# Kernel tuning notes

Measured on AMD Instinct MI355X. Metric: run time of the kernel, lower is better.

## Reference

```python
import jax, jax.numpy as jnp
import numpy as np

N_EMBED = 1024
N_HEAD = 16
SEQ = 2048
BATCH = 2


def setup_inputs() -> dict:
    key = jax.random.key(0)
    ks = jax.random.split(key, 5)
    scale_in = 1.0 / np.sqrt(N_EMBED)
    x = jax.random.normal(ks[0], (BATCH, SEQ, N_EMBED), dtype=jnp.float32)
    # attn_proj: Linear(n_embed, 3*n_embed); stored as [in, out] so y = x @ W + b
    W_qkv = jax.random.normal(ks[1], (N_EMBED, 3 * N_EMBED), dtype=jnp.float32) * scale_in
    b_qkv = jax.random.normal(ks[2], (3 * N_EMBED,), dtype=jnp.float32) * 0.01
    # fin_proj: Linear(n_embed, n_embed)
    W_out = jax.random.normal(ks[3], (N_EMBED, N_EMBED), dtype=jnp.float32) * scale_in
    b_out = jax.random.normal(ks[4], (N_EMBED,), dtype=jnp.float32) * 0.01
    return {"x": x, "W_qkv": W_qkv, "b_qkv": b_qkv, "W_out": W_out, "b_out": b_out}


def reference(x, W_qkv, b_qkv, W_out, b_out):
    B, S, D = x.shape
    H = N_HEAD
    hd = D // H
    qkv = x @ W_qkv + b_qkv  # [B, S, 3D]
    q, k, v = jnp.split(qkv, 3, axis=-1)
    # [B, H, S, hd]
    q = q.reshape(B, S, H, hd).transpose(0, 2, 1, 3)
    k = k.reshape(B, S, H, hd).transpose(0, 2, 1, 3)
    v = v.reshape(B, S, H, hd).transpose(0, 2, 1, 3)
    scores = jnp.einsum("bhqd,bhkd->bhqk", q, k) * (1.0 / np.sqrt(hd))
    causal = jnp.tril(jnp.ones((S, S), dtype=bool))  # lower-triangular mask
    scores = jnp.where(causal[None, None], scores, -jnp.inf)
    probs = jax.nn.softmax(scores, axis=-1)
    # dropout is identity in eval mode (inference reference)
    attn = jnp.einsum("bhqk,bhkd->bhqd", probs, v)  # [B, H, S, hd]
    attn = attn.transpose(0, 2, 1, 3).reshape(B, S, D)
    return attn @ W_out + b_out
```

## Files before the change

kernel.cpp:

```cpp
#include <hip/hip_runtime.h>

typedef short bf16x8 __attribute__((ext_vector_type(8)));
typedef short bf16x4 __attribute__((ext_vector_type(4)));
typedef float f32x4 __attribute__((ext_vector_type(4)));
typedef int i32x4 __attribute__((ext_vector_type(4)));
typedef int i32x2 __attribute__((ext_vector_type(2)));

#define MFMA16x16x32(a, b, c) __builtin_amdgcn_mfma_f32_16x16x32_bf16(a, b, c, 0, 0, 0)
#define TRR(dst, a) asm volatile("ds_read_b64_tr_b16 %0, %1" : "=v"(dst) : "v"(a))

__device__ __forceinline__ unsigned short f2bf(float f) {
  union { float f; unsigned u; } v; v.f = f;
  unsigned u = v.u + 0x7FFFu + ((v.u >> 16) & 1u);
  return (unsigned short)(u >> 16);
}

__device__ __forceinline__ unsigned cvtpk(float lo, float hi) {
  unsigned r;
  asm("v_cvt_pk_bf16_f32 %0, %1, %2" : "=v"(r) : "v"(lo), "v"(hi));
  return r;
}

__device__ __forceinline__ float max3f(float a, float b, float c) {
  float d;
  asm("v_max3_f32 %0, %1, %2, %3" : "=v"(d) : "v"(a), "v"(b), "v"(c));
  return d;
}

__device__ __forceinline__ void gload16(const void* g, void* l) {
  __builtin_amdgcn_global_load_lds((const __attribute__((address_space(1))) void*)g,
                                   (__attribute__((address_space(3))) void*)l, 16, 0, 0);
}

__device__ __forceinline__ unsigned ldsoff(const void* p) {
  return (unsigned)(unsigned long long)(const __attribute__((address_space(3))) void*)p;
}

__global__ __launch_bounds__(256) void conv_bf16(const float* __restrict__ in,
                                                 unsigned short* __restrict__ out, int n8) {
  int i = blockIdx.x * 256 + threadIdx.x;
  if (i >= n8) return;
  const float4* p = reinterpret_cast<const float4*>(in + (long)i * 8);
  float4 a = p[0], b = p[1];
  i32x4 o;
  o[0] = cvtpk(a.x, a.y); o[1] = cvtpk(a.z, a.w);
  o[2] = cvtpk(b.x, b.y); o[3] = cvtpk(b.z, b.w);
  *reinterpret_cast<i32x4*>(out + (long)i * 8) = o;
}

__global__ __launch_bounds__(256) void trans_f32_bf16(const float* __restrict__ W,
                                                      unsigned short* __restrict__ Wt,
                                                      int K, int N) {
  __shared__ float tile[32][33];
  int n0 = blockIdx.x << 5, k0 = blockIdx.y << 5;
  int tx = threadIdx.x, ty = threadIdx.y;
#pragma unroll
  for (int i = 0; i < 32; i += 8)
    tile[ty + i][tx] = W[(long)(k0 + ty + i) * N + n0 + tx];
  __syncthreads();
#pragma unroll
  for (int i = 0; i < 32; i += 8)
    Wt[(long)(n0 + ty + i) * K + k0 + tx] = f2bf(tile[tx][ty + i]);
}

template <int BF16OUT>
__global__ __launch_bounds__(256) void gemm_bt(const unsigned short* __restrict__ A,
                                               const unsigned short* __restrict__ Bt,
                                               const float* __restrict__ bias,
                                               void* __restrict__ Cv,
                                               int M, int N, int K) {
  __shared__ __align__(128) unsigned short As[4096];
  __shared__ __align__(128) unsigned short Bs[4096];
  int t = threadIdx.x;
  int w = t >> 6, l = t & 63;
  int g = l >> 4, m16 = l & 15;
  int wr = w >> 1, wc = w & 1;
  long am0 = (long)blockIdx.y << 7;
  long bn0 = (long)blockIdx.x << 7;
  f32x4 acc[4][4];
#pragma unroll
  for (int i = 0; i < 4; ++i)
#pragma unroll
    for (int j = 0; j < 4; ++j) acc[i][j] = (f32x4){0.f, 0.f, 0.f, 0.f};

  for (int k0 = 0; k0 < K; k0 += 32) {
#pragma unroll
    for (int i = 0; i < 2; ++i) {
      int seg = i * 4 + w;
      int flat = (seg << 9) + (l << 3);
      int r_ = flat >> 5, c_ = flat & 31;
      gload16(A + (am0 + r_) * K + k0 + c_, &As[seg << 9]);
      gload16(Bt + (bn0 + r_) * K + k0 + c_, &Bs[seg << 9]);
    }
    __syncthreads();
    bf16x8 af[4], bfr[4];
#pragma unroll
    for (int im = 0; im < 4; ++im)
      af[im] = *(const bf16x8*)&As[((wr << 6) + (im << 4) + m16) * 32 + (g << 3)];
#pragma unroll
    for (int in = 0; in < 4; ++in)
      bfr[in] = *(const bf16x8*)&Bs[((wc << 6) + (in << 4) + m16) * 32 + (g << 3)];
    __builtin_amdgcn_s_setprio(1);
#pragma unroll
    for (int im = 0; im < 4; ++im)
#pragma unroll
      for (int in = 0; in < 4; ++in)
        acc[im][in] = MFMA16x16x32(af[im], bfr[in], acc[im][in]);
    __builtin_amdgcn_s_setprio(0);
    __syncthreads();
  }

#pragma unroll
  for (int im = 0; im < 4; ++im) {
#pragma unroll
    for (int in = 0; in < 4; ++in) {
      long col = bn0 + (wc << 6) + (in << 4) + m16;
      float bval = bias[col];
#pragma unroll
      for (int r = 0; r < 4; ++r) {
        long row = am0 + (wr << 6) + (im << 4) + (g << 2) + r;
        float v = acc[im][in][r] + bval;
        if (BF16OUT)
          ((unsigned short*)Cv)[row * N + col] = f2bf(v);
        else
          ((float*)Cv)[row * N + col] = v;
      }
    }
  }
}

__global__ __launch_bounds__(256) void attn_fwd(const unsigned short* __restrict__ qkv,
                                                unsigned short* __restrict__ out) {
  const int D3 = 3072;
  const float C1 = 0.18033688f;
  const float THR = 11.5415603f;
  __shared__ __align__(128) unsigned short Ks[2][4096];
  __shared__ __align__(128) unsigned short Vs[2][4096];
  int b = blockIdx.x >> 4, h = blockIdx.x & 15;
  int t = threadIdx.x;
  int w = t >> 6, l = t & 63;
  int g = l >> 4, m16 = l & 15;
  long base = (long)b * 2048 * D3;
  const unsigned short* kbase = qkv + base + 1024 + h * 64;
  const unsigned short* vbase = qkv + base + 2048 + h * 64;

  int l8 = l >> 3, sc = l & 7;
  int kof = (w * 8 + l8) * D3 + ((sc ^ l8) << 3);
  int s0 = w * 8 + l8;
  int vof = ((s0 & 15) * 4 + (sc >> 1)) * D3 + ((s0 >> 4) << 4) + ((sc & 1) << 3);
  const f32x4 zero4 = (f32x4){0.f, 0.f, 0.f, 0.f};

  for (int sgi = 0; sgi < 2; ++sgi) {
    int qt = sgi ? (31 - blockIdx.y) : blockIdx.y;
    int q0 = qt << 6;
    int qrow = q0 + (w << 4) + m16;
    const unsigned short* qp = qkv + base + (long)qrow * D3 + h * 64;
    bf16x8 qf0 = *(const bf16x8*)(qp + g * 8);
    bf16x8 qf1 = *(const bf16x8*)(qp + 32 + g * 8);

    f32x4 O[4];
#pragma unroll
    for (int d = 0; d < 4; ++d) O[d] = zero4;
    float m2 = -1e30f, lsum = 0.f;
    int nt = qt + 1;

    gload16(kbase + kof, &Ks[0][w << 9]);
    gload16(kbase + 32 * D3 + kof, &Ks[0][2048 + (w << 9)]);
    gload16(vbase + vof, &Vs[0][w << 9]);
    gload16(vbase + vof + 32, &Vs[0][2048 + (w << 9)]);
    __syncthreads();

    int buf = 0;
    for (int it = 0; it < nt; ++it) {
      if (it + 1 < nt) {
        long off = (long)(it + 1) * 64 * D3;
        gload16(kbase + off + kof, &Ks[buf ^ 1][w << 9]);
        gload16(kbase + off + 32 * D3 + kof, &Ks[buf ^ 1][2048 + (w << 9)]);
        gload16(vbase + off + vof, &Vs[buf ^ 1][w << 9]);
        gload16(vbase + off + vof + 32, &Vs[buf ^ 1][2048 + (w << 9)]);
      }
      unsigned va = ldsoff(&Vs[buf][0]) + (g << 7) + (m16 << 3);
      bf16x4 t0[4], t1[4], t2[4], t3[4];
#pragma unroll
      for (int d = 0; d < 4; ++d) {
        unsigned a = va + (d << 11);
        TRR(t0[d], a);
        TRR(t1[d], a + 512);
        TRR(t2[d], a + 1024);
        TRR(t3[d], a + 1536);
      }
      const char* kbuf = (const char*)&Ks[buf][0];
      int swz = m16 & 7;
      bf16x8 kf0[4], kf1[4];
#pragma unroll
      for (int T = 0; T < 4; ++T) {
        const char* rp = kbuf + (((T << 4) + m16) << 7);
        kf0[T] = *(const bf16x8*)(rp + ((g ^ swz) << 4));
        kf1[T] = *(const bf16x8*)(rp + (((4 + g) ^ swz) << 4));
      }
      f32x4 st[4];
      __builtin_amdgcn_s_setprio(1);
#pragma unroll
      for (int T = 0; T < 4; ++T) {
        st[T] = MFMA16x16x32(kf0[T], qf0, zero4);
        st[T] = MFMA16x16x32(kf1[T], qf1, st[T]);
      }
      __builtin_amdgcn_s_setprio(0);

      if (it == nt - 1) {
        int rq = (w << 4) + m16;
#pragma unroll
        for (int T = 0; T < 4; ++T)
#pragma unroll
          for (int r = 0; r < 4; ++r)
            if ((T << 4) + (g << 2) + r > rq) st[T][r] = -3e38f;
      }
      float tmax = max3f(st[0][0], st[0][1], st[0][2]);
      tmax = max3f(tmax, st[0][3], st[1][0]);
      tmax = max3f(tmax, st[1][1], st[1][2]);
      tmax = max3f(tmax, st[1][3], st[2][0]);
      tmax = max3f(tmax, st[2][1], st[2][2]);
      tmax = max3f(tmax, st[2][3], st[3][0]);
      tmax = max3f(tmax, st[3][1], st[3][2]);
      tmax = fmaxf(tmax, st[3][3]);
      tmax = fmaxf(tmax, __shfl_xor(tmax, 16));
      tmax = fmaxf(tmax, __shfl_xor(tmax, 32));
      float tsc2 = tmax * C1;
      bool skip = __all(tsc2 <= m2 + THR);
      float mnew2 = skip ? m2 : fmaxf(m2, tsc2);
      float p[4][4];
      float tsum = 0.f;
#pragma unroll
      for (int T = 0; T < 4; ++T)
#pragma unroll
        for (int r = 0; r < 4; ++r) {
          float e = __builtin_amdgcn_exp2f(fmaf(st[T][r], C1, -mnew2));
          p[T][r] = e;
          tsum += e;
        }
      tsum += __shfl_xor(tsum, 16);
      tsum += __shfl_xor(tsum, 32);
      if (!skip) {
        float alpha = __builtin_amdgcn_exp2f(m2 - mnew2);
        lsum *= alpha;
#pragma unroll
        for (int d = 0; d < 4; ++d) {
          O[d][0] *= alpha; O[d][1] *= alpha; O[d][2] *= alpha; O[d][3] *= alpha;
        }
        m2 = mnew2;
      }
      lsum += tsum;

      i32x4 w0, w1;
      w0[0] = cvtpk(p[0][0], p[0][1]); w0[1] = cvtpk(p[0][2], p[0][3]);
      w0[2] = cvtpk(p[1][0], p[1][1]); w0[3] = cvtpk(p[1][2], p[1][3]);
      w1[0] = cvtpk(p[2][0], p[2][1]); w1[1] = cvtpk(p[2][2], p[2][3]);
      w1[2] = cvtpk(p[3][0], p[3][1]); w1[3] = cvtpk(p[3][2], p[3][3]);
      bf16x8 pb0 = __builtin_bit_cast(bf16x8, w0);
      bf16x8 pb1 = __builtin_bit_cast(bf16x8, w1);

      asm volatile("s_waitcnt lgkmcnt(0)" ::: "memory");
      __builtin_amdgcn_sched_barrier(0);

      bf16x8 vfA[4], vfB[4];
#pragma unroll
      for (int d = 0; d < 4; ++d) {
        vfA[d] = __builtin_shufflevector(t0[d], t1[d], 0, 1, 2, 3, 4, 5, 6, 7);
        vfB[d] = __builtin_shufflevector(t2[d], t3[d], 0, 1, 2, 3, 4, 5, 6, 7);
      }
      __builtin_amdgcn_s_setprio(1);
#pragma unroll
      for (int d = 0; d < 4; ++d) {
        O[d] = MFMA16x16x32(vfA[d], pb0, O[d]);
        O[d] = MFMA16x16x32(vfB[d], pb1, O[d]);
      }
      __builtin_amdgcn_s_setprio(0);
      __syncthreads();
      buf ^= 1;
    }

    float inv = 1.0f / lsum;
    unsigned short* op = out + (long)(b * 2048 + qrow) * 1024 + h * 64;
#pragma unroll
    for (int d = 0; d < 4; ++d) {
      i32x2 pk;
      pk[0] = (int)cvtpk(O[d][0] * inv, O[d][1] * inv);
      pk[1] = (int)cvtpk(O[d][2] * inv, O[d][3] * inv);
      *reinterpret_cast<i32x2*>(op + (d << 4) + (g << 2)) = pk;
    }
  }
}

extern "C" void kernel_launch(void* const* d_in, const int* in_sizes, int n_in,
                              void* d_out, int out_size, void* d_ws, size_t ws_size,
                              hipStream_t stream) {
  const float* x     = (const float*)d_in[0];
  const float* W_qkv = (const float*)d_in[1];
  const float* b_qkv = (const float*)d_in[2];
  const float* W_out = (const float*)d_in[3];
  const float* b_out = (const float*)d_in[4];

  char* ws = (char*)d_ws;
  unsigned short* xb    = (unsigned short*)ws;
  unsigned short* wqkvT = (unsigned short*)(ws + (8l << 20));
  unsigned short* woutT = (unsigned short*)(ws + (14l << 20));
  unsigned short* qkv   = (unsigned short*)(ws + (16l << 20));

  conv_bf16<<<2048, 256, 0, stream>>>(x, xb, 524288);
  trans_f32_bf16<<<dim3(96, 32), dim3(32, 8), 0, stream>>>(W_qkv, wqkvT, 1024, 3072);
  trans_f32_bf16<<<dim3(32, 32), dim3(32, 8), 0, stream>>>(W_out, woutT, 1024, 1024);
  gemm_bt<1><<<dim3(24, 32), 256, 0, stream>>>(xb, wqkvT, b_qkv, (void*)qkv, 4096, 3072, 1024);
  attn_fwd<<<dim3(32, 16), 256, 0, stream>>>(qkv, xb);
  gemm_bt<0><<<dim3(8, 32), 256, 0, stream>>>(xb, woutT, b_out, d_out, 4096, 1024, 1024);
}
```

Baseline: 119.0 us.

## Widen attention KV tile to 128 keys per iteration

Doubles the key/value tile processed per loop iteration from 64 to 128 rows, with double-buffered shared memory grown to match and the V staging layout changed to suit. This halves the number of iterations and block-wide barriers per query tile and amortizes softmax reductions over more scores. It also sets launch bounds to request two blocks per CU. The costs are more LDS and registers per block, and more masked work on the diagonal tile, since a 64-row query tile now meets a 128-key tile.

```diff
diff --git a/kernel.cpp b/kernel.cpp
--- a/kernel.cpp
+++ b/kernel.cpp
@@ -129,13 +129,13 @@
   }
 }
 
-__global__ __launch_bounds__(256) void attn_fwd(const unsigned short* __restrict__ qkv,
-                                                unsigned short* __restrict__ out) {
+__global__ __launch_bounds__(256, 2) void attn_fwd(const unsigned short* __restrict__ qkv,
+                                                   unsigned short* __restrict__ out) {
   const int D3 = 3072;
   const float C1 = 0.18033688f;
   const float THR = 11.5415603f;
-  __shared__ __align__(128) unsigned short Ks[2][4096];
-  __shared__ __align__(128) unsigned short Vs[2][4096];
+  __shared__ __align__(128) unsigned short Ks[2][8192];
+  __shared__ __align__(128) unsigned short Vs[2][8192];
   int b = blockIdx.x >> 4, h = blockIdx.x & 15;
   int t = threadIdx.x;
   int w = t >> 6, l = t & 63;
@@ -146,8 +146,7 @@
 
   int l8 = l >> 3, sc = l & 7;
   int kof = (w * 8 + l8) * D3 + ((sc ^ l8) << 3);
-  int s0 = w * 8 + l8;
-  int vof = ((s0 & 15) * 4 + (sc >> 1)) * D3 + ((s0 >> 4) << 4) + ((sc & 1) << 3);
+  int vof = ((w * 8 + l8) * 4 + (sc >> 1)) * D3 + ((sc & 1) << 3);
   const f32x4 zero4 = (f32x4){0.f, 0.f, 0.f, 0.f};
 
   for (int sgi = 0; sgi < 2; ++sgi) {
@@ -162,82 +161,80 @@
 #pragma unroll
     for (int d = 0; d < 4; ++d) O[d] = zero4;
     float m2 = -1e30f, lsum = 0.f;
-    int nt = qt + 1;
-
-    gload16(kbase + kof, &Ks[0][w << 9]);
-    gload16(kbase + 32 * D3 + kof, &Ks[0][2048 + (w << 9)]);
-    gload16(vbase + vof, &Vs[0][w << 9]);
-    gload16(vbase + vof + 32, &Vs[0][2048 + (w << 9)]);
+    int nt = (qt >> 1) + 1;
+
+#pragma unroll
+    for (int i = 0; i < 4; ++i) {
+      gload16(kbase + kof + i * 32 * D3, &Ks[0][(i << 11) + (w << 9)]);
+      gload16(vbase + vof + (i << 4), &Vs[0][(i << 11) + (w << 9)]);
+    }
     __syncthreads();
 
     int buf = 0;
     for (int it = 0; it < nt; ++it) {
       if (it + 1 < nt) {
-        long off = (long)(it + 1) * 64 * D3;
-        gload16(kbase + off + kof, &Ks[buf ^ 1][w << 9]);
-        gload16(kbase + off + 32 * D3 + kof, &Ks[buf ^ 1][2048 + (w << 9)]);
-        gload16(vbase + off + vof, &Vs[buf ^ 1][w << 9]);
-        gload16(vbase + off + vof + 32, &Vs[buf ^ 1][2048 + (w << 9)]);
+        long off = (long)(it + 1) * 128 * D3;
+#pragma unroll
+        for (int i = 0; i < 4; ++i) {
+          gload16(kbase + off + kof + i * 32 * D3, &Ks[buf ^ 1][(i << 11) + (w << 9)]);
+          gload16(vbase + off + vof + (i << 4), &Vs[buf ^ 1][(i << 11) + (w << 9)]);
+        }
       }
       unsigned va = ldsoff(&Vs[buf][0]) + (g << 7) + (m16 << 3);
-      bf16x4 t0[4], t1[4], t2[4], t3[4];
-#pragma unroll
-      for (int d = 0; d < 4; ++d) {
-        unsigned a = va + (d << 11);
-        TRR(t0[d], a);
-        TRR(t1[d], a + 512);
-        TRR(t2[d], a + 1024);
-        TRR(t3[d], a + 1536);
-      }
+      bf16x4 tLo[4][4], tHi[4][4];
+#pragma unroll
+      for (int G = 0; G < 4; ++G)
+#pragma unroll
+        for (int d = 0; d < 4; ++d) {
+          unsigned a = va + (G << 10) + (d << 12);
+          TRR(tLo[G][d], a);
+          TRR(tHi[G][d], a + 512);
+        }
       const char* kbuf = (const char*)&Ks[buf][0];
       int swz = m16 & 7;
-      bf16x8 kf0[4], kf1[4];
-#pragma unroll
-      for (int T = 0; T < 4; ++T) {
+      f32x4 st[8];
+      __builtin_amdgcn_s_setprio(1);
+#pragma unroll
+      for (int T = 0; T < 8; ++T) {
         const char* rp = kbuf + (((T << 4) + m16) << 7);
-        kf0[T] = *(const bf16x8*)(rp + ((g ^ swz) << 4));
-        kf1[T] = *(const bf16x8*)(rp + (((4 + g) ^ swz) << 4));
-      }
-      f32x4 st[4];
-      __builtin_amdgcn_s_setprio(1);
-#pragma unroll
-      for (int T = 0; T < 4; ++T) {
-        st[T] = MFMA16x16x32(kf0[T], qf0, zero4);
-        st[T] = MFMA16x16x32(kf1[T], qf1, st[T]);
+        bf16x8 kf0 = *(const bf16x8*)(rp + ((g ^ swz) << 4));
+        bf16x8 kf1 = *(const bf16x8*)(rp + (((4 + g) ^ swz) << 4));
+        st[T] = MFMA16x16x32(kf0, qf0, zero4);
+        st[T] = MFMA16x16x32(kf1, qf1, st[T]);
       }
       __builtin_amdgcn_s_setprio(0);
 
       if (it == nt - 1) {
-        int rq = (w << 4) + m16;
-#pragma unroll
-        for (int T = 0; T < 4; ++T)
+        int rq = qrow - (it << 7);
+#pragma unroll
+        for (int T = 0; T < 8; ++T)
 #pragma unroll
           for (int r = 0; r < 4; ++r)
             if ((T << 4) + (g << 2) + r > rq) st[T][r] = -3e38f;
       }
-      float tmax = max3f(st[0][0], st[0][1], st[0][2]);
-      tmax = max3f(tmax, st[0][3], st[1][0]);
-      tmax = max3f(tmax, st[1][1], st[1][2]);
-      tmax = max3f(tmax, st[1][3], st[2][0]);
-      tmax = max3f(tmax, st[2][1], st[2][2]);
-      tmax = max3f(tmax, st[2][3], st[3][0]);
-      tmax = max3f(tmax, st[3][1], st[3][2]);
-      tmax = fmaxf(tmax, st[3][3]);
+      float tm[8];
+#pragma unroll
+      for (int T = 0; T < 8; ++T)
+        tm[T] = max3f(fmaxf(st[T][0], st[T][1]), st[T][2], st[T][3]);
+      float u0 = max3f(tm[0], tm[1], tm[2]);
+      float u1 = max3f(tm[3], tm[4], tm[5]);
+      float tmax = max3f(u0, u1, fmaxf(tm[6], tm[7]));
       tmax = fmaxf(tmax, __shfl_xor(tmax, 16));
       tmax = fmaxf(tmax, __shfl_xor(tmax, 32));
       float tsc2 = tmax * C1;
       bool skip = __all(tsc2 <= m2 + THR);
       float mnew2 = skip ? m2 : fmaxf(m2, tsc2);
-      float p[4][4];
-      float tsum = 0.f;
-#pragma unroll
-      for (int T = 0; T < 4; ++T)
+      float p[8][4];
+      f32x4 ts4 = zero4;
+#pragma unroll
+      for (int T = 0; T < 8; ++T)
 #pragma unroll
         for (int r = 0; r < 4; ++r) {
           float e = __builtin_amdgcn_exp2f(fmaf(st[T][r], C1, -mnew2));
           p[T][r] = e;
-          tsum += e;
-        }
+          ts4[r] += e;
+        }
+      float tsum = (ts4[0] + ts4[1]) + (ts4[2] + ts4[3]);
       tsum += __shfl_xor(tsum, 16);
       tsum += __shfl_xor(tsum, 32);
       if (!skip) {
@@ -251,29 +248,28 @@
       }
       lsum += tsum;
 
-      i32x4 w0, w1;
-      w0[0] = cvtpk(p[0][0], p[0][1]); w0[1] = cvtpk(p[0][2], p[0][3]);
-      w0[2] = cvtpk(p[1][0], p[1][1]); w0[3] = cvtpk(p[1][2], p[1][3]);
-      w1[0] = cvtpk(p[2][0], p[2][1]); w1[1] = cvtpk(p[2][2], p[2][3]);
-      w1[2] = cvtpk(p[3][0], p[3][1]); w1[3] = cvtpk(p[3][2], p[3][3]);
-      bf16x8 pb0 = __builtin_bit_cast(bf16x8, w0);
-      bf16x8 pb1 = __builtin_bit_cast(bf16x8, w1);
+      bf16x8 pb[4];
+#pragma unroll
+      for (int G = 0; G < 4; ++G) {
+        i32x4 wv;
+        wv[0] = cvtpk(p[2 * G][0], p[2 * G][1]);
+        wv[1] = cvtpk(p[2 * G][2], p[2 * G][3]);
+        wv[2] = cvtpk(p[2 * G + 1][0], p[2 * G + 1][1]);
+        wv[3] = cvtpk(p[2 * G + 1][2], p[2 * G + 1][3]);
+        pb[G] = __builtin_bit_cast(bf16x8, wv);
+      }
 
       asm volatile("s_waitcnt lgkmcnt(0)" ::: "memory");
       __builtin_amdgcn_sched_barrier(0);
 
-      bf16x8 vfA[4], vfB[4];
-#pragma unroll
-      for (int d = 0; d < 4; ++d) {
-        vfA[d] = __builtin_shufflevector(t0[d], t1[d], 0, 1, 2, 3, 4, 5, 6, 7);
-        vfB[d] = __builtin_shufflevector(t2[d], t3[d], 0, 1, 2, 3, 4, 5, 6, 7);
-      }
       __builtin_amdgcn_s_setprio(1);
 #pragma unroll
-      for (int d = 0; d < 4; ++d) {
-        O[d] = MFMA16x16x32(vfA[d], pb0, O[d]);
-        O[d] = MFMA16x16x32(vfB[d], pb1, O[d]);
-      }
+      for (int d = 0; d < 4; ++d)
+#pragma unroll
+        for (int G = 0; G < 4; ++G) {
+          bf16x8 vf = __builtin_shufflevector(tLo[G][d], tHi[G][d], 0, 1, 2, 3, 4, 5, 6, 7);
+          O[d] = MFMA16x16x32(vf, pb[G], O[d]);
+        }
       __builtin_amdgcn_s_setprio(0);
       __syncthreads();
       buf ^= 1;
```

Measured after the change: 118.2 us. No clear change (-0.7%).
